# Kernel tuning notes

Measured on AMD Instinct MI355X. Metric: run time of the kernel, lower is better.

## Reference

```python
import jax, jax.numpy as jnp
import numpy as np

B, S, H, NH, DH, F, L = 4, 2048, 512, 8, 64, 2048, 4
ALPHA = 1.0   # config.lag_time_scale_alpha
EPS = 1e-12   # BERT layer_norm_eps
MS_PER_MIN = 60.0 * 1000.0


def setup_inputs() -> dict:
    key = jax.random.key(0)
    ks = jax.random.split(key, 24)
    p = lambda k, shape: (jax.random.normal(k, shape, jnp.float32) * 0.02)
    inp = {
        "query_states": jax.random.normal(ks[0], (B, S, H), jnp.float32),
        "attention_mask": jnp.zeros((B, 1, 1, S), jnp.float32),
        "position_bias": jax.random.normal(ks[1], (1, NH, S, S), jnp.float32) * 0.02,
        "timestamp": jnp.sort(jax.random.randint(ks[2], (B, S), 0, 36_000_000, jnp.int32), axis=-1),
        # stacked per-layer parameters (L leading dim)
        "wq": p(ks[3], (L, H, H)), "bq": jnp.zeros((L, H), jnp.float32),
        "wk": p(ks[4], (L, H, H)), "bk": jnp.zeros((L, H), jnp.float32),
        "wv": p(ks[5], (L, H, H)), "bv": jnp.zeros((L, H), jnp.float32),
        "wo": p(ks[6], (L, H, H)), "bo": jnp.zeros((L, H), jnp.float32),
        "ln1_g": jnp.ones((L, H), jnp.float32), "ln1_b": jnp.zeros((L, H), jnp.float32),
        "wi": p(ks[7], (L, H, F)), "bi": jnp.zeros((L, F), jnp.float32),
        "wo2": p(ks[8], (L, F, H)), "bo2": jnp.zeros((L, H), jnp.float32),
        "ln2_g": jnp.ones((L, H), jnp.float32), "ln2_b": jnp.zeros((L, H), jnp.float32),
    }
    return inp


def _ln(x, g, b):
    m = x.mean(-1, keepdims=True)
    v = ((x - m) ** 2).mean(-1, keepdims=True)
    return (x - m) / jnp.sqrt(v + EPS) * g + b


def reference(query_states, attention_mask, position_bias, timestamp,
              wq, bq, wk, bk, wv, bv, wo, bo, ln1_g, ln1_b,
              wi, bi, wo2, bo2, ln2_g, ln2_b):
    # encoder (is_decoder=False) lag-time scale: (B,1,S,S)
    lag = (timestamp[:, None, :, None] - timestamp[:, None, None, :]).astype(jnp.float32) / MS_PER_MIN
    scale = np.sqrt(DH).astype(np.float32) - ALPHA / (jnp.clip(lag, 0.0) + 1.0) + ALPHA

    x = query_states
    for l in range(L):
        def proj(w, b):
            return (x @ w + b).reshape(B, S, NH, DH).transpose(0, 2, 1, 3)  # (B,NH,S,DH)
        q, k, v = proj(wq[l], bq[l]), proj(wk[l], bk[l]), proj(wv[l], bv[l])
        scores = jnp.einsum('bhqd,bhkd->bhqk', q, k) / scale + position_bias + attention_mask
        probs = jax.nn.softmax(scores, axis=-1)
        ctx = jnp.einsum('bhqk,bhkd->bhqd', probs, v).transpose(0, 2, 1, 3).reshape(B, S, H)
        attn = _ln(ctx @ wo[l] + bo[l] + x, ln1_g[l], ln1_b[l])
        ffn = jax.nn.gelu(attn @ wi[l] + bi[l], approximate=False) @ wo2[l] + bo2[l]
        x = _ln(ffn + attn, ln2_g[l], ln2_b[l])
    return x
```

## Files before the change

### kernel.cpp

```cpp
#include <hip/hip_runtime.h>
#include <stdint.h>

typedef unsigned short u16;
using half8   = __attribute__((ext_vector_type(8))) _Float16;
using float4v = __attribute__((ext_vector_type(4))) float;

#define L2E 1.4426950408889634f

__device__ inline float4v f4zero() { float4v z = {0.f, 0.f, 0.f, 0.f}; return z; }

__device__ inline u16 f2h(float f) {
  union { _Float16 h; u16 u; } v; v.h = (_Float16)f; return v.u;
}
__device__ inline float h2f(u16 u) {
  union { u16 u; _Float16 h; } v; v.u = u; return (float)v.h;
}

__device__ inline void glds16(const u16* g, u16* lds_base, int lane) {
#if __has_builtin(__builtin_amdgcn_global_load_lds)
  (void)lane;
  __builtin_amdgcn_global_load_lds((const __attribute__((address_space(1))) void*)g,
                                   (__attribute__((address_space(3))) void*)lds_base,
                                   16, 0, 0);
#else
  *(uint4*)(lds_base + (size_t)lane * 8) = *(const uint4*)g;
#endif
}

__global__ __launch_bounds__(256) void transpose_cast_kernel(
    const float* __restrict__ in, u16* __restrict__ out, int K, int N, size_t out_ls) {
  __shared__ float tile[32][33];
  const int tx = threadIdx.x & 31, ty = threadIdx.x >> 5;
  in  += (size_t)blockIdx.z * K * N;
  out += (size_t)blockIdx.z * out_ls;
  const int n  = blockIdx.x * 32 + tx;
  const int k0 = blockIdx.y * 32;
#pragma unroll
  for (int j = 0; j < 32; j += 8)
    tile[ty + j][tx] = in[(size_t)(k0 + ty + j) * N + n];
  __syncthreads();
  const int k = k0 + tx;
  const int n0 = blockIdx.x * 32;
#pragma unroll
  for (int j = 0; j < 32; j += 8)
    out[(size_t)(n0 + ty + j) * K + k] = f2h(tile[tx][ty + j]);
}

__global__ __launch_bounds__(256) void cast_kernel(const float* __restrict__ in,
                                                   u16* __restrict__ out) {
  const int i = (blockIdx.x * 256 + threadIdx.x) * 4;
  float4 t = *(const float4*)(in + i);
  ushort4 o;
  o.x = f2h(t.x); o.y = f2h(t.y); o.z = f2h(t.z); o.w = f2h(t.w);
  *(ushort4*)(out + i) = o;
}

__global__ __launch_bounds__(256) void pb_tile_kernel(const float* __restrict__ pb,
                                                      u16* __restrict__ pbT) {
  const int g  = blockIdx.x * 256 + threadIdx.x;
  const int mm = g & 15;
  const int q  = (g >> 4) & 2047;
  const int kbh = g >> 15;
  const int kb = kbh & 31, h = kbh >> 5;
  const float* src = pb + ((size_t)h * 2048 + q) * 2048 + kb * 64 + mm;
  ushort4 o;
  o.x = f2h(src[0]  * L2E);
  o.y = f2h(src[16] * L2E);
  o.z = f2h(src[32] * L2E);
  o.w = f2h(src[48] * L2E);
  *(ushort4*)(pbT + ((size_t)(h * 32 + kb) * 2048 + q) * 64 + mm * 4) = o;
}

__global__ __launch_bounds__(256) void inv_tile_kernel(const int* __restrict__ ts,
                                                       u16* __restrict__ invT) {
  const int g  = blockIdx.x * 256 + threadIdx.x;
  const int mm = g & 15;
  const int q  = (g >> 4) & 2047;
  const int kb = (g >> 15) & 31;
  const int b  = g >> 20;
  const int tq = ts[b * 2048 + q];
  ushort4 o;
  u16* op = (u16*)&o;
#pragma unroll
  for (int nb = 0; nb < 4; nb++) {
    const int k = kb * 64 + nb * 16 + mm;
    const int du = tq - ts[b * 2048 + k];
    const float u = (du > 0) ? (float)du : 0.f;
    op[nb] = f2h(fmaf(u, L2E, 86561.70245333781f) *
                 __builtin_amdgcn_rcpf(fmaf(u, 9.f, 480000.f)));
  }
  *(ushort4*)(invT + ((size_t)(b * 32 + kb) * 2048 + q) * 64 + mm * 4) = o;
}

__global__ __launch_bounds__(256) void maskts_kernel(const float* __restrict__ mask,
                                                     const int* __restrict__ ts,
                                                     float* __restrict__ maskE,
                                                     float* __restrict__ tsf) {
  const int i = blockIdx.x * 256 + threadIdx.x;
  maskE[i] = mask[i] * L2E;
  tsf[i]   = (float)ts[i];
}

template <int BM, int BN, int NN, int KK, int EPI>
__global__ __launch_bounds__(256) void gemm_kernel(
    const u16* __restrict__ A, const u16* __restrict__ Wt,
    const float* __restrict__ b0, const float* __restrict__ b1, const float* __restrict__ b2,
    const u16* __restrict__ resid,
    void* __restrict__ o0, void* __restrict__ o1, void* __restrict__ o2) {
  constexpr int FI = BM / 32;
  constexpr int FJB = BN / 32;
  constexpr int FIW = BM / 32;
  constexpr int FJW = BN / 32;
  __shared__ __align__(16) u16 As[BM * 64];
  __shared__ __align__(16) u16 Bs[BN * 64];
  const int tid = threadIdx.x, lane = tid & 63, wv = tid >> 6;
  const int quad = lane >> 4, mm = lane & 15;
  const int m0 = blockIdx.x * BM, n0 = blockIdx.y * BN;
  const int wm = (wv >> 1) * (BM / 2), wn = (wv & 1) * (BN / 2);
  const int srow = tid >> 3, slot = tid & 7;
  const int chunk = slot ^ (srow & 7);
  const u16* Ag = A  + (size_t)(m0 + srow) * KK + chunk * 8;
  const u16* Bg = Wt + (size_t)(n0 + srow) * KK + chunk * 8;
  u16* AsW = As + (size_t)(wv * 8) * 64;
  u16* BsW = Bs + (size_t)(wv * 8) * 64;
  const int sw = mm & 7;

  float4v acc[FIW][FJW];
#pragma unroll
  for (int i = 0; i < FIW; i++)
#pragma unroll
    for (int j = 0; j < FJW; j++) acc[i][j] = f4zero();

  for (int kt = 0; kt < KK; kt += 64) {
#pragma unroll
    for (int i = 0; i < FI; i++)
      glds16(Ag + (size_t)i * 32 * KK + kt, AsW + i * 32 * 64, lane);
#pragma unroll
    for (int j = 0; j < FJB; j++)
      glds16(Bg + (size_t)j * 32 * KK + kt, BsW + j * 32 * 64, lane);
    __syncthreads();
#pragma unroll
    for (int ks = 0; ks < 2; ks++) {
      half8 a[FIW], b[FJW];
#pragma unroll
      for (int i = 0; i < FIW; i++)
        a[i] = *(const half8*)(As + (size_t)(wm + i * 16 + mm) * 64 + (size_t)((ks * 4 + quad) ^ sw) * 8);
#pragma unroll
      for (int j = 0; j < FJW; j++)
        b[j] = *(const half8*)(Bs + (size_t)(wn + j * 16 + mm) * 64 + (size_t)((ks * 4 + quad) ^ sw) * 8);
#pragma unroll
      for (int i = 0; i < FIW; i++)
#pragma unroll
        for (int j = 0; j < FJW; j++)
          acc[i][j] = __builtin_amdgcn_mfma_f32_16x16x32_f16(a[i], b[j], acc[i][j], 0, 0, 0);
    }
    __syncthreads();
  }

#pragma unroll
  for (int j = 0; j < FJW; j++) {
    const int gn = n0 + wn + j * 16 + mm;
    if (EPI == 4) {
      const int which = gn >> 9, col = gn & 511, h = (gn >> 6) & 7, d = gn & 63;
      const float* bp = (which == 0) ? b0 : (which == 1) ? b1 : b2;
      const float bias = bp[col];
      u16* dst = (which == 0) ? (u16*)o0 : (which == 1) ? (u16*)o1 : (u16*)o2;
#pragma unroll
      for (int i = 0; i < FIW; i++)
#pragma unroll
        for (int r = 0; r < 4; r++) {
          const int gm = m0 + wm + i * 16 + quad * 4 + r;
          const int b_ = gm >> 11, s_ = gm & 2047;
          const float val = acc[i][j][r] + bias;
          if (which < 2)
            dst[((size_t)((b_ * 8 + h) * 2048 + s_)) * 64 + d] = f2h(val);
          else
            dst[((size_t)((b_ * 8 + h) * 64 + d)) * 2048 + s_] = f2h(val);
        }
    } else {
      const float bias = b0[gn];
#pragma unroll
      for (int i = 0; i < FIW; i++)
#pragma unroll
        for (int r = 0; r < 4; r++) {
          const int gm = m0 + wm + i * 16 + quad * 4 + r;
          const float val = acc[i][j][r] + bias;
          const size_t idx = (size_t)gm * NN + gn;
          if (EPI == 2) {
            ((float*)o0)[idx] = val + h2f(resid[idx]);
          } else {
            const float z  = val * 0.70710678118654752f;
            const float az = fabsf(z);
            const float t  = __builtin_amdgcn_rcpf(1.0f + 0.3275911f * az);
            const float poly = t * (0.254829592f + t * (-0.284496736f +
                               t * (1.421413741f + t * (-1.453152027f + t * 1.061405429f))));
            const float e = __builtin_amdgcn_exp2f(-az * az * L2E);
            float erf_ = 1.0f - poly * e;
            erf_ = (z < 0.0f) ? -erf_ : erf_;
            ((u16*)o0)[idx] = f2h(val * 0.5f * (1.0f + erf_));
          }
        }
    }
  }
}

template <int TILED>
__global__ __launch_bounds__(256) void flash4_kernel(
    const u16* __restrict__ Q, const u16* __restrict__ Kb, const u16* __restrict__ Vt,
    const u16* __restrict__ pbT, const u16* __restrict__ invT,
    const float* __restrict__ pb32,
    const float* __restrict__ maskE, const float* __restrict__ tsf,
    u16* __restrict__ ctx) {
  __shared__ __align__(16) u16 Kls[64 * 64];
  __shared__ __align__(16) u16 Vls[64 * 64];
  __shared__ __align__(16) u16 P[4][16 * 72];
  const int tid = threadIdx.x, lane = tid & 63, w = tid >> 6;
  const int quad = lane >> 4, mm = lane & 15;
  const int bh = blockIdx.y, b_ = bh >> 3, h_ = bh & 7;
  const int q0 = blockIdx.x * 64 + w * 16;
  const size_t qk_base = (size_t)bh * 2048 * 64;
  const size_t v_base  = (size_t)bh * 64 * 2048;
  const int srow = lane >> 3, slot = lane & 7;
  const int chunk = slot ^ srow;
  const int sw = mm & 7;

  half8 aq[2];
#pragma unroll
  for (int t = 0; t < 2; t++)
    aq[t] = *(const half8*)(Q + qk_base + (size_t)(q0 + mm) * 64 + t * 32 + quad * 8);

  float tqf[4];
  if (TILED < 2) {
#pragma unroll
    for (int r = 0; r < 4; r++) tqf[r] = tsf[b_ * 2048 + q0 + quad * 4 + r];
  }

  float l_r[4] = {0.f, 0.f, 0.f, 0.f};
  float4v o[4];
#pragma unroll
  for (int ob = 0; ob < 4; ob++) o[ob] = f4zero();

  ushort4 pbc[4], invc[4]; float tkc[4], mkc[4];
  if (TILED >= 1) {
#pragma unroll
    for (int r = 0; r < 4; r++)
      pbc[r] = *(const ushort4*)(pbT + ((size_t)(h_ * 32) * 2048 + q0 + quad * 4 + r) * 64 + mm * 4);
  }
  if (TILED == 2) {
#pragma unroll
    for (int r = 0; r < 4; r++)
      invc[r] = *(const ushort4*)(invT + ((size_t)(b_ * 32) * 2048 + q0 + quad * 4 + r) * 64 + mm * 4);
  } else {
#pragma unroll
    for (int nb = 0; nb < 4; nb++) tkc[nb] = tsf[b_ * 2048 + nb * 16 + mm];
  }
#pragma unroll
  for (int nb = 0; nb < 4; nb++) mkc[nb] = maskE[b_ * 2048 + nb * 16 + mm];

  for (int kt = 0; kt < 32; kt++) {
    const int k0 = kt * 64;
    __syncthreads();
#pragma unroll
    for (int i = 0; i < 2; i++) {
      const int row = w * 16 + i * 8 + srow;
      glds16(Kb + qk_base + (size_t)(k0 + row) * 64 + chunk * 8, Kls + (w * 16 + i * 8) * 64, lane);
      glds16(Vt + v_base + (size_t)row * 2048 + k0 + chunk * 8, Vls + (w * 16 + i * 8) * 64, lane);
    }
    __syncthreads();

    float4v s[4];
#pragma unroll
    for (int nb = 0; nb < 4; nb++) {
      const half8 kf0 = *(const half8*)(Kls + (size_t)(nb * 16 + mm) * 64 + (size_t)(quad ^ sw) * 8);
      const half8 kf1 = *(const half8*)(Kls + (size_t)(nb * 16 + mm) * 64 + (size_t)((4 + quad) ^ sw) * 8);
      s[nb] = __builtin_amdgcn_mfma_f32_16x16x32_f16(aq[0], kf0, f4zero(), 0, 0, 0);
      s[nb] = __builtin_amdgcn_mfma_f32_16x16x32_f16(aq[1], kf1, s[nb], 0, 0, 0);
    }

    const int kn = (kt < 31) ? kt + 1 : kt;
    ushort4 pbn[4], invn[4]; float tkn[4], mkn[4];
    if (TILED >= 1) {
#pragma unroll
      for (int r = 0; r < 4; r++)
        pbn[r] = *(const ushort4*)(pbT + ((size_t)(h_ * 32 + kn) * 2048 + q0 + quad * 4 + r) * 64 + mm * 4);
    }
    if (TILED == 2) {
#pragma unroll
      for (int r = 0; r < 4; r++)
        invn[r] = *(const ushort4*)(invT + ((size_t)(b_ * 32 + kn) * 2048 + q0 + quad * 4 + r) * 64 + mm * 4);
    } else {
#pragma unroll
      for (int nb = 0; nb < 4; nb++) tkn[nb] = tsf[b_ * 2048 + kn * 64 + nb * 16 + mm];
    }
#pragma unroll
    for (int nb = 0; nb < 4; nb++) mkn[nb] = maskE[b_ * 2048 + kn * 64 + nb * 16 + mm];

#pragma unroll
    for (int r = 0; r < 4; r++) {
      float pbv[4], iv[4];
      if (TILED >= 1) {
        pbv[0] = h2f(pbc[r].x); pbv[1] = h2f(pbc[r].y);
        pbv[2] = h2f(pbc[r].z); pbv[3] = h2f(pbc[r].w);
      } else {
#pragma unroll
        for (int nb = 0; nb < 4; nb++)
          pbv[nb] = pb32[((size_t)h_ * 2048 + q0 + quad * 4 + r) * 2048 + k0 + nb * 16 + mm] * L2E;
      }
      if (TILED == 2) {
        iv[0] = h2f(invc[r].x); iv[1] = h2f(invc[r].y);
        iv[2] = h2f(invc[r].z); iv[3] = h2f(invc[r].w);
      } else {
#pragma unroll
        for (int nb = 0; nb < 4; nb++) {
          const float u = fmaxf(tqf[r] - tkc[nb], 0.f);
          iv[nb] = fmaf(u, L2E, 86561.70245333781f) *
                   __builtin_amdgcn_rcpf(fmaf(u, 9.f, 480000.f));
        }
      }
#pragma unroll
      for (int nb = 0; nb < 4; nb++) {
        const float t = fmaf(s[nb][r], iv[nb], pbv[nb] + mkc[nb]);
        const float p = __builtin_amdgcn_exp2f(t);
        l_r[r] += p;
        P[w][(quad * 4 + r) * 72 + nb * 16 + mm] = f2h(p);
      }
    }

    const half8 ap0 = *(const half8*)(&P[w][mm * 72 + quad * 8]);
    const half8 ap1 = *(const half8*)(&P[w][mm * 72 + 32 + quad * 8]);
#pragma unroll
    for (int ob = 0; ob < 4; ob++) {
      const half8 vf0 = *(const half8*)(Vls + (size_t)(ob * 16 + mm) * 64 + (size_t)(quad ^ sw) * 8);
      const half8 vf1 = *(const half8*)(Vls + (size_t)(ob * 16 + mm) * 64 + (size_t)((4 + quad) ^ sw) * 8);
      o[ob] = __builtin_amdgcn_mfma_f32_16x16x32_f16(ap0, vf0, o[ob], 0, 0, 0);
      o[ob] = __builtin_amdgcn_mfma_f32_16x16x32_f16(ap1, vf1, o[ob], 0, 0, 0);
    }
#pragma unroll
    for (int r = 0; r < 4; r++) { pbc[r] = pbn[r]; invc[r] = invn[r]; }
#pragma unroll
    for (int nb = 0; nb < 4; nb++) { tkc[nb] = tkn[nb]; mkc[nb] = mkn[nb]; }
  }

#pragma unroll
  for (int r = 0; r < 4; r++) {
    float l = l_r[r];
#pragma unroll
    for (int sh = 1; sh < 16; sh <<= 1) l += __shfl_xor(l, sh, 64);
    const float rl = __builtin_amdgcn_rcpf(l);
    const int qrow = q0 + quad * 4 + r;
#pragma unroll
    for (int ob = 0; ob < 4; ob++)
      ctx[((size_t)b_ * 2048 + qrow) * 512 + h_ * 64 + ob * 16 + mm] = f2h(o[ob][r] * rl);
  }
}

__global__ __launch_bounds__(256) void ln_kernel(
    const float* __restrict__ in, const float* __restrict__ g, const float* __restrict__ bb,
    float* __restrict__ of, u16* __restrict__ obf) {
  const int lane = threadIdx.x & 63, w = threadIdx.x >> 6;
  const int row = blockIdx.x * 4 + w;
  const float* x = in + (size_t)row * 512;
  float v[8];
  const float4 t0 = *(const float4*)(x + lane * 8);
  const float4 t1 = *(const float4*)(x + lane * 8 + 4);
  v[0] = t0.x; v[1] = t0.y; v[2] = t0.z; v[3] = t0.w;
  v[4] = t1.x; v[5] = t1.y; v[6] = t1.z; v[7] = t1.w;
  float s = 0.f;
#pragma unroll
  for (int i = 0; i < 8; i++) s += v[i];
#pragma unroll
  for (int sh = 1; sh < 64; sh <<= 1) s += __shfl_xor(s, sh, 64);
  const float mean = s * (1.0f / 512.0f);
  float sq = 0.f;
#pragma unroll
  for (int i = 0; i < 8; i++) { const float d = v[i] - mean; sq += d * d; }
#pragma unroll
  for (int sh = 1; sh < 64; sh <<= 1) sq += __shfl_xor(sq, sh, 64);
  const float rstd = rsqrtf(sq * (1.0f / 512.0f) + 1e-12f);
#pragma unroll
  for (int i = 0; i < 8; i++) {
    const int col = lane * 8 + i;
    const float y = (v[i] - mean) * rstd * g[col] + bb[col];
    if (of) of[(size_t)row * 512 + col] = y;
    obf[(size_t)row * 512 + col] = f2h(y);
  }
}

extern "C" void kernel_launch(void* const* d_in, const int* in_sizes, int n_in,
                              void* d_out, int out_size, void* d_ws, size_t ws_size,
                              hipStream_t stream) {
  const float* x_in = (const float*)d_in[0];
  const float* mask = (const float*)d_in[1];
  const float* pb   = (const float*)d_in[2];
  const int*   ts   = (const int*)d_in[3];
  const float* wq = (const float*)d_in[4];  const float* bq = (const float*)d_in[5];
  const float* wk = (const float*)d_in[6];  const float* bk = (const float*)d_in[7];
  const float* wvp = (const float*)d_in[8]; const float* bv = (const float*)d_in[9];
  const float* wo = (const float*)d_in[10]; const float* bo = (const float*)d_in[11];
  const float* ln1g = (const float*)d_in[12]; const float* ln1b = (const float*)d_in[13];
  const float* wi = (const float*)d_in[14]; const float* bi = (const float*)d_in[15];
  const float* wo2 = (const float*)d_in[16]; const float* bo2 = (const float*)d_in[17];
  const float* ln2g = (const float*)d_in[18]; const float* ln2b = (const float*)d_in[19];

  char* ws = (char*)d_ws;
  const size_t o_wqkv  = 0;
  const size_t o_woT   = 6291456;
  const size_t o_wiT   = 8388608;
  const size_t o_wo2T  = 16777216;
  const size_t o_maskE = 25165824;
  const size_t o_tsf   = 25198592;
  const size_t o_xbf   = 25231360;
  const size_t o_qb    = 33619968;
  const size_t o_kb    = 42008576;
  const size_t o_vb    = 50397184;
  const size_t o_ctx   = 58785792;
  const size_t o_attnb = 67174400;
  const size_t o_tmp   = 75563008;
  const size_t o_pbT   = 92340224;
  const size_t o_invT  = 159449088;
  const int tiled = (ws_size >= o_invT + 33554432ull) ? 2
                  : (ws_size >= o_pbT + 67108864ull) ? 1 : 0;

  u16*   wqkvT = (u16*)(ws + o_wqkv);
  u16*   woT   = (u16*)(ws + o_woT);
  u16*   wiT   = (u16*)(ws + o_wiT);
  u16*   wo2T  = (u16*)(ws + o_wo2T);
  float* maskE = (float*)(ws + o_maskE);
  float* tsf   = (float*)(ws + o_tsf);
  u16*   xbf   = (u16*)(ws + o_xbf);
  u16*   qb    = (u16*)(ws + o_qb);
  u16*   kb    = (u16*)(ws + o_kb);
  u16*   vb    = (u16*)(ws + o_vb);
  u16*   ctx   = (u16*)(ws + o_ctx);
  u16*   hb    = (u16*)(ws + o_qb);
  u16*   attnb = (u16*)(ws + o_attnb);
  float* tmp   = (float*)(ws + o_tmp);
  u16*   pbT   = (u16*)(ws + o_pbT);
  u16*   invT  = (u16*)(ws + o_invT);

  const dim3 blk(256);
  transpose_cast_kernel<<<dim3(16, 16, 4), blk, 0, stream>>>(wq,  wqkvT,          512, 512, 786432);
  transpose_cast_kernel<<<dim3(16, 16, 4), blk, 0, stream>>>(wk,  wqkvT + 262144, 512, 512, 786432);
  transpose_cast_kernel<<<dim3(16, 16, 4), blk, 0, stream>>>(wvp, wqkvT + 524288, 512, 512, 786432);
  transpose_cast_kernel<<<dim3(16, 16, 4), blk, 0, stream>>>(wo,  woT,  512, 512,  262144);
  transpose_cast_kernel<<<dim3(64, 16, 4), blk, 0, stream>>>(wi,  wiT,  512, 2048, 1048576);
  transpose_cast_kernel<<<dim3(16, 64, 4), blk, 0, stream>>>(wo2, wo2T, 2048, 512, 1048576);
  maskts_kernel<<<32, blk, 0, stream>>>(mask, ts, maskE, tsf);
  cast_kernel<<<4096, blk, 0, stream>>>(x_in, xbf);
  if (tiled >= 1) pb_tile_kernel<<<32768, blk, 0, stream>>>(pb, pbT);
  if (tiled == 2) inv_tile_kernel<<<16384, blk, 0, stream>>>(ts, invT);

  for (int l = 0; l < 4; l++) {
    gemm_kernel<128, 128, 1536, 512, 4><<<dim3(64, 12), blk, 0, stream>>>(
        xbf, wqkvT + (size_t)l * 786432, bq + l * 512, bk + l * 512, bv + l * 512,
        nullptr, qb, kb, vb);
    if (tiled == 2)
      flash4_kernel<2><<<dim3(32, 32), blk, 0, stream>>>(qb, kb, vb, pbT, invT, pb, maskE, tsf, ctx);
    else if (tiled == 1)
      flash4_kernel<1><<<dim3(32, 32), blk, 0, stream>>>(qb, kb, vb, pbT, nullptr, pb, maskE, tsf, ctx);
    else
      flash4_kernel<0><<<dim3(32, 32), blk, 0, stream>>>(qb, kb, vb, nullptr, nullptr, pb, maskE, tsf, ctx);
    gemm_kernel<128, 64, 512, 512, 2><<<dim3(64, 8), blk, 0, stream>>>(
        ctx, woT + (size_t)l * 262144, bo + l * 512, nullptr, nullptr, xbf,
        tmp, nullptr, nullptr);
    ln_kernel<<<2048, blk, 0, stream>>>(tmp, ln1g + l * 512, ln1b + l * 512, nullptr, attnb);
    gemm_kernel<128, 128, 2048, 512, 3><<<dim3(64, 16), blk, 0, stream>>>(
        attnb, wiT + (size_t)l * 1048576, bi + l * 2048, nullptr, nullptr, nullptr,
        hb, nullptr, nullptr);
    gemm_kernel<128, 64, 512, 2048, 2><<<dim3(64, 8), blk, 0, stream>>>(
        hb, wo2T + (size_t)l * 1048576, bo2 + l * 512, nullptr, nullptr, attnb,
        tmp, nullptr, nullptr);
    ln_kernel<<<2048, blk, 0, stream>>>(tmp, ln2g + l * 512, ln2b + l * 512,
                                        (l == 3) ? (float*)d_out : nullptr, xbf);
  }
  (void)in_sizes; (void)n_in; (void)out_size;
}
```

Baseline: 1.364 ms.

## Double-buffer K/V tiles in LDS and do softmax math in packed fp16

The attention kernel now double-buffers the K and V tiles in LDS. The loads for the next key tile are issued before the current tile is computed, which removes one barrier per iteration and hides global-load latency. The scale, bias and exp2 arithmetic moves to packed fp16 (pkrtz conversion, half2 fma, v_exp_f16, and fdot2 for the row sums), cutting VALU work. The P tile is repacked without padding using an XOR swizzle and 4-wide stores, so the QKV epilogue writes V with a matching column permutation inside each 64-block. This trades accuracy in the exponent and score path for fewer instructions, and the code depends on the permuted V layout matching the P layout exactly.

```diff
diff --git a/kernel.cpp b/kernel.cpp
--- a/kernel.cpp
+++ b/kernel.cpp
@@ -3,6 +3,8 @@
 
 typedef unsigned short u16;
 using half8   = __attribute__((ext_vector_type(8))) _Float16;
+using half4v  = __attribute__((ext_vector_type(4))) _Float16;
+using half2v  = __attribute__((ext_vector_type(2))) _Float16;
 using float4v = __attribute__((ext_vector_type(4))) float;
 
 #define L2E 1.4426950408889634f
@@ -14,6 +16,24 @@
 }
 __device__ inline float h2f(u16 u) {
   union { u16 u; _Float16 h; } v; v.u = u; return (float)v.h;
+}
+
+__device__ inline half2v cvtpk(float a, float b) {
+  return __builtin_bit_cast(half2v, __builtin_amdgcn_cvt_pkrtz(a, b));
+}
+__device__ inline _Float16 hexp2_(_Float16 x) {
+  _Float16 r;
+  asm("v_exp_f16 %0, %1" : "=v"(r) : "v"(x));
+  return r;
+}
+__device__ inline float fdot2f(half2v a, float c) {
+#if __has_builtin(__builtin_amdgcn_fdot2)
+  typedef __attribute__((ext_vector_type(2))) __fp16 h2r;
+  return __builtin_amdgcn_fdot2(__builtin_bit_cast(h2r, a),
+                                __builtin_bit_cast(h2r, 0x3C003C00u), c, false);
+#else
+  return c + (float)a.x + (float)a.y;
+#endif
 }
 
 __device__ inline void glds16(const u16* g, u16* lds_base, int lane) {
@@ -175,7 +195,8 @@
           if (which < 2)
             dst[((size_t)((b_ * 8 + h) * 2048 + s_)) * 64 + d] = f2h(val);
           else
-            dst[((size_t)((b_ * 8 + h) * 64 + d)) * 2048 + s_] = f2h(val);
+            dst[((size_t)((b_ * 8 + h) * 64 + d)) * 2048 +
+                (s_ & ~63) + (((s_ & 15) << 2) | ((s_ >> 4) & 3))] = f2h(val);
         }
     } else {
       const float bias = b0[gn];
@@ -211,9 +232,9 @@
     const float* __restrict__ pb32,
     const float* __restrict__ maskE, const float* __restrict__ tsf,
     u16* __restrict__ ctx) {
-  __shared__ __align__(16) u16 Kls[64 * 64];
-  __shared__ __align__(16) u16 Vls[64 * 64];
-  __shared__ __align__(16) u16 P[4][16 * 72];
+  __shared__ __align__(16) u16 Kls[2][64 * 64];
+  __shared__ __align__(16) u16 Vls[2][64 * 64];
+  __shared__ __align__(16) u16 P[4][16 * 64];
   const int tid = threadIdx.x, lane = tid & 63, w = tid >> 6;
   const int quad = lane >> 4, mm = lane & 15;
   const int bh = blockIdx.y, b_ = bh >> 3, h_ = bh & 7;
@@ -224,6 +245,19 @@
   const int chunk = slot ^ srow;
   const int sw = mm & 7;
 
+  const u16* Kgl = Kb + qk_base + (size_t)(w * 16 + srow) * 64 + chunk * 8;
+  const u16* Vgl = Vt + v_base + (size_t)(w * 16 + srow) * 2048 + chunk * 8;
+
+  {
+    u16* kd = &Kls[0][(w * 16) * 64];
+    u16* vd = &Vls[0][(w * 16) * 64];
+#pragma unroll
+    for (int i = 0; i < 2; i++) {
+      glds16(Kgl + (size_t)i * 512, kd + i * 8 * 64, lane);
+      glds16(Vgl + (size_t)i * 8 * 2048, vd + i * 8 * 64, lane);
+    }
+  }
+
   half8 aq[2];
 #pragma unroll
   for (int t = 0; t < 2; t++)
@@ -257,22 +291,29 @@
 #pragma unroll
   for (int nb = 0; nb < 4; nb++) mkc[nb] = maskE[b_ * 2048 + nb * 16 + mm];
 
+  int cur = 0;
   for (int kt = 0; kt < 32; kt++) {
     const int k0 = kt * 64;
     __syncthreads();
-#pragma unroll
-    for (int i = 0; i < 2; i++) {
-      const int row = w * 16 + i * 8 + srow;
-      glds16(Kb + qk_base + (size_t)(k0 + row) * 64 + chunk * 8, Kls + (w * 16 + i * 8) * 64, lane);
-      glds16(Vt + v_base + (size_t)row * 2048 + k0 + chunk * 8, Vls + (w * 16 + i * 8) * 64, lane);
-    }
-    __syncthreads();
-
+
+    if (kt < 31) {
+      u16* kd = &Kls[cur ^ 1][(w * 16) * 64];
+      u16* vd = &Vls[cur ^ 1][(w * 16) * 64];
+      const size_t ko = (size_t)(kt + 1) * 4096;
+      const size_t vo = (size_t)(kt + 1) * 64;
+#pragma unroll
+      for (int i = 0; i < 2; i++) {
+        glds16(Kgl + ko + (size_t)i * 512, kd + i * 8 * 64, lane);
+        glds16(Vgl + vo + (size_t)i * 8 * 2048, vd + i * 8 * 64, lane);
+      }
+    }
+
+    const u16* Kc = Kls[cur];
     float4v s[4];
 #pragma unroll
     for (int nb = 0; nb < 4; nb++) {
-      const half8 kf0 = *(const half8*)(Kls + (size_t)(nb * 16 + mm) * 64 + (size_t)(quad ^ sw) * 8);
-      const half8 kf1 = *(const half8*)(Kls + (size_t)(nb * 16 + mm) * 64 + (size_t)((4 + quad) ^ sw) * 8);
+      const half8 kf0 = *(const half8*)(Kc + (size_t)(nb * 16 + mm) * 64 + (size_t)(quad ^ sw) * 8);
+      const half8 kf1 = *(const half8*)(Kc + (size_t)(nb * 16 + mm) * 64 + (size_t)((4 + quad) ^ sw) * 8);
       s[nb] = __builtin_amdgcn_mfma_f32_16x16x32_f16(aq[0], kf0, f4zero(), 0, 0, 0);
       s[nb] = __builtin_amdgcn_mfma_f32_16x16x32_f16(aq[1], kf1, s[nb], 0, 0, 0);
     }
@@ -295,43 +336,58 @@
 #pragma unroll
     for (int nb = 0; nb < 4; nb++) mkn[nb] = maskE[b_ * 2048 + kn * 64 + nb * 16 + mm];
 
+    const half2v mk01 = cvtpk(mkc[0], mkc[1]);
+    const half2v mk23 = cvtpk(mkc[2], mkc[3]);
 #pragma unroll
     for (int r = 0; r < 4; r++) {
-      float pbv[4], iv[4];
+      half2v pb01, pb23, iv01, iv23;
       if (TILED >= 1) {
-        pbv[0] = h2f(pbc[r].x); pbv[1] = h2f(pbc[r].y);
-        pbv[2] = h2f(pbc[r].z); pbv[3] = h2f(pbc[r].w);
+        pb01 = *(const half2v*)&pbc[r].x;
+        pb23 = *(const half2v*)&pbc[r].z;
       } else {
+        float pv[4];
 #pragma unroll
         for (int nb = 0; nb < 4; nb++)
-          pbv[nb] = pb32[((size_t)h_ * 2048 + q0 + quad * 4 + r) * 2048 + k0 + nb * 16 + mm] * L2E;
+          pv[nb] = pb32[((size_t)h_ * 2048 + q0 + quad * 4 + r) * 2048 + k0 + nb * 16 + mm] * L2E;
+        pb01 = cvtpk(pv[0], pv[1]); pb23 = cvtpk(pv[2], pv[3]);
       }
       if (TILED == 2) {
-        iv[0] = h2f(invc[r].x); iv[1] = h2f(invc[r].y);
-        iv[2] = h2f(invc[r].z); iv[3] = h2f(invc[r].w);
+        iv01 = *(const half2v*)&invc[r].x;
+        iv23 = *(const half2v*)&invc[r].z;
       } else {
+        float ivv[4];
 #pragma unroll
         for (int nb = 0; nb < 4; nb++) {
           const float u = fmaxf(tqf[r] - tkc[nb], 0.f);
-          iv[nb] = fmaf(u, L2E, 86561.70245333781f) *
-                   __builtin_amdgcn_rcpf(fmaf(u, 9.f, 480000.f));
+          ivv[nb] = fmaf(u, L2E, 86561.70245333781f) *
+                    __builtin_amdgcn_rcpf(fmaf(u, 9.f, 480000.f));
         }
+        iv01 = cvtpk(ivv[0], ivv[1]); iv23 = cvtpk(ivv[2], ivv[3]);
       }
-#pragma unroll
-      for (int nb = 0; nb < 4; nb++) {
-        const float t = fmaf(s[nb][r], iv[nb], pbv[nb] + mkc[nb]);
-        const float p = __builtin_amdgcn_exp2f(t);
-        l_r[r] += p;
-        P[w][(quad * 4 + r) * 72 + nb * 16 + mm] = f2h(p);
-      }
-    }
-
-    const half8 ap0 = *(const half8*)(&P[w][mm * 72 + quad * 8]);
-    const half8 ap1 = *(const half8*)(&P[w][mm * 72 + 32 + quad * 8]);
+      const half2v s01 = cvtpk(s[0][r], s[1][r]);
+      const half2v s23 = cvtpk(s[2][r], s[3][r]);
+      const half2v t01 = __builtin_elementwise_fma(s01, iv01, pb01 + mk01);
+      const half2v t23 = __builtin_elementwise_fma(s23, iv23, pb23 + mk23);
+      half2v p01, p23;
+      p01.x = hexp2_(t01.x); p01.y = hexp2_(t01.y);
+      p23.x = hexp2_(t23.x); p23.y = hexp2_(t23.y);
+      l_r[r] = fdot2f(p01, l_r[r]);
+      l_r[r] = fdot2f(p23, l_r[r]);
+      const int prow = quad * 4 + r;
+      union { half2v h2[2]; half4v h4; } uu;
+      uu.h2[0] = p01; uu.h2[1] = p23;
+      *(half4v*)((char*)P[w] + prow * 128 + ((mm * 8) ^ ((prow & 7) << 4))) = uu.h4;
+    }
+
+    const u16* Vc = Vls[cur];
+    const char* Pb = (const char*)P[w] + mm * 128;
+    const int pxor = (mm & 7) << 4;
+    const half8 ap0 = *(const half8*)(Pb + ((quad * 16) ^ pxor));
+    const half8 ap1 = *(const half8*)(Pb + ((64 + quad * 16) ^ pxor));
 #pragma unroll
     for (int ob = 0; ob < 4; ob++) {
-      const half8 vf0 = *(const half8*)(Vls + (size_t)(ob * 16 + mm) * 64 + (size_t)(quad ^ sw) * 8);
-      const half8 vf1 = *(const half8*)(Vls + (size_t)(ob * 16 + mm) * 64 + (size_t)((4 + quad) ^ sw) * 8);
+      const half8 vf0 = *(const half8*)(Vc + (size_t)(ob * 16 + mm) * 64 + (size_t)(quad ^ sw) * 8);
+      const half8 vf1 = *(const half8*)(Vc + (size_t)(ob * 16 + mm) * 64 + (size_t)((4 + quad) ^ sw) * 8);
       o[ob] = __builtin_amdgcn_mfma_f32_16x16x32_f16(ap0, vf0, o[ob], 0, 0, 0);
       o[ob] = __builtin_amdgcn_mfma_f32_16x16x32_f16(ap1, vf1, o[ob], 0, 0, 0);
     }
@@ -339,6 +395,7 @@
     for (int r = 0; r < 4; r++) { pbc[r] = pbn[r]; invc[r] = invn[r]; }
 #pragma unroll
     for (int nb = 0; nb < 4; nb++) { tkc[nb] = tkn[nb]; mkc[nb] = mkn[nb]; }
+    cur ^= 1;
   }
 
 #pragma unroll
```

After: 1.400 ms. 2.6% more time.
